# Optimization experiments

Measured on AMD Instinct MI355X. Metric: run time of the kernel, lower is better.

## Reference

```python
import jax, jax.numpy as jnp
import numpy as np

B, S, D, H = 4, 2048, 1024, 16
DK = D // H
THETA = 10000.0


def setup_inputs() -> dict:
    key = jax.random.key(0)
    ks = jax.random.split(key, 5)
    std = (2.0 / (D + D)) ** 0.5  # Linear init std (distribution differs from trunc-normal; math identical)
    x = jax.random.normal(ks[0], (B, S, D), dtype=jnp.float32)
    wq = jax.random.normal(ks[1], (D, D), dtype=jnp.float32) * std
    wk = jax.random.normal(ks[2], (D, D), dtype=jnp.float32) * std
    wv = jax.random.normal(ks[3], (D, D), dtype=jnp.float32) * std
    wo = jax.random.normal(ks[4], (D, D), dtype=jnp.float32) * std
    mask = jnp.tril(jnp.ones((S, S), dtype=bool))  # causal
    return {"x": x, "mask": mask, "wq": wq, "wk": wk, "wv": wv, "wo": wo}


def _rope(t):
    # t: [b, h, s, dk]; interleaved pairs (even, odd)
    s = t.shape[-2]
    inv_freq = THETA ** (-jnp.arange(0, DK, 2, dtype=jnp.float32) / DK)  # [dk/2]
    ang = jnp.arange(s, dtype=jnp.float32)[:, None] * inv_freq[None, :]  # [s, dk/2]
    cos = jnp.cos(ang)[None, None, :, :]
    sin = jnp.sin(ang)[None, None, :, :]
    x1 = t[..., 0::2]
    x2 = t[..., 1::2]
    rot = jnp.stack([x1 * cos - x2 * sin, x1 * sin + x2 * cos], axis=-1)
    return rot.reshape(t.shape)


def reference(x, mask, wq, wk, wv, wo):
    b, s, d = x.shape
    def heads(w):
        return jnp.einsum('bsd,ed->bse', x, w).reshape(b, s, H, DK).transpose(0, 2, 1, 3)
    q = _rope(heads(wq))
    k = _rope(heads(wk))
    v = heads(wv)
    scores = jnp.einsum('bhqd,bhkd->bhqk', q, k) / (DK ** 0.5)
    scores = jnp.where(mask, scores, -jnp.inf)
    attn = jax.nn.softmax(scores, axis=-1)
    out = jnp.einsum('bhqk,bhkd->bhqd', attn, v)
    out = out.transpose(0, 2, 1, 3).reshape(b, s, d)
    return jnp.einsum('bsd,ed->bse', out, wo)
```

## Files before the change

kernel.cpp:

```cpp
#include <hip/hip_runtime.h>

constexpr int Bc = 4, Sc = 2048, Dc = 1024, Hc = 16, DKc = 64;
constexpr int Mc = Bc * Sc;

typedef __bf16 bf16x8 __attribute__((ext_vector_type(8)));
typedef float f32x4 __attribute__((ext_vector_type(4)));
typedef unsigned short ush;

#define DEVI __device__ __forceinline__

DEVI ush bf(float f) { return __builtin_bit_cast(ush, (__bf16)f); }

DEVI void ld_lds16(const void* g, void* l) {
    __builtin_amdgcn_global_load_lds(
        (const __attribute__((address_space(1))) unsigned int*)g,
        (__attribute__((address_space(3))) unsigned int*)l,
        16, 0, 0);
}

constexpr unsigned CVT_BLOCKS = 6144;
constexpr unsigned TAB_BLOCKS = 32;

__global__ __launch_bounds__(256) void cvt_all(
    const float* __restrict__ x,  const float* __restrict__ wq,
    const float* __restrict__ wk, const float* __restrict__ wv,
    const float* __restrict__ wo, ush* __restrict__ dst,
    float2* __restrict__ csn)
{
    if (blockIdx.x >= CVT_BLOCKS) {
        int t = (int)(blockIdx.x - CVT_BLOCKS) * 256 + threadIdx.x;
#pragma unroll
        for (int i = 0; i < 8; i++) {
            int idx = t * 8 + i;
            int s = idx >> 5, p = idx & 31;
            float ang = (float)s * exp2f(-(float)p * 0.4152410118609203f);
            csn[idx] = make_float2(cosf(ang), sinf(ang));
        }
        return;
    }
    size_t t = ((size_t)blockIdx.x * 256 + threadIdx.x) * 8;
    const float* src; size_t loc;
    const size_t NX = (size_t)Mc * Dc;
    if (t < NX) { src = x; loc = t; }
    else {
        size_t u = t - NX;
        int wi = (int)(u >> 20);
        src = (wi == 0) ? wq : ((wi == 1) ? wk : ((wi == 2) ? wv : wo));
        loc = u & 1048575u;
    }
    float4 a = *(const float4*)(src + loc);
    float4 b = *(const float4*)(src + loc + 4);
    union { ush u[8]; float4 v; } o;
    o.u[0] = bf(a.x); o.u[1] = bf(a.y); o.u[2] = bf(a.z); o.u[3] = bf(a.w);
    o.u[4] = bf(b.x); o.u[5] = bf(b.y); o.u[6] = bf(b.z); o.u[7] = bf(b.w);
    *(float4*)(dst + t) = o.v;
}

template<int MODE>
__global__ __launch_bounds__(256) void gemm_bf(
    const ush* __restrict__ A,
    const ush* __restrict__ W0, const ush* __restrict__ W1,
    const ush* __restrict__ W2,
    ush* __restrict__ Oq, ush* __restrict__ Ok, ush* __restrict__ Ovt,
    float* __restrict__ Of, const float2* __restrict__ csn)
{
    __shared__ ush sA[128 * 64];
    __shared__ ush sB[128 * 64];

    const int xcd = (int)blockIdx.x;
    const int u = (int)blockIdx.y + 64 * (int)blockIdx.z;
    const int z = (MODE == 0) ? (u >> 6) : 0;
    const int w = u & 63;
    const int m0 = (xcd * 8 + (w >> 3)) * 128;
    const int n0 = (w & 7) * 128;

    const ush* W = (z == 0) ? W0 : ((z == 1) ? W1 : W2);

    const int tid = threadIdx.x;
    const int wv = tid >> 6;
    const int ln = tid & 63;
    const int lr = ln & 15;
    const int lq = ln >> 4;
    const int wm = (wv & 1) * 64;
    const int wn = (wv >> 1) * 64;
    const int rL = ln >> 3;
    const int cSw = ((ln & 7) ^ rL) * 8;
    const int ca0 = lq ^ (ln & 7);

    f32x4 acc[4][4] = {};
    const bool swp = (MODE == 0) && (z == 2);

    for (int kt = 0; kt < 1024; kt += 64) {
        __syncthreads();
#pragma unroll
        for (int i = 0; i < 4; i++) {
            int chunk = wv * 4 + i;
            int rr = chunk * 8 + rL;
            ld_lds16(&A[(size_t)(m0 + rr) * 1024 + kt + cSw], &sA[chunk * 512]);
            ld_lds16(&W[(size_t)(n0 + rr) * 1024 + kt + cSw], &sB[chunk * 512]);
        }
        __syncthreads();
#pragma unroll
        for (int ks = 0; ks < 2; ks++) {
            const int cf = (ca0 ^ (ks << 2)) << 3;
            bf16x8 af[4], bfr[4];
#pragma unroll
            for (int t = 0; t < 4; t++) {
                af[t]  = *(const bf16x8*)(&sA[(wm + t * 16 + lr) * 64 + cf]);
                bfr[t] = *(const bf16x8*)(&sB[(wn + t * 16 + lr) * 64 + cf]);
            }
            __builtin_amdgcn_s_setprio(1);
            if (!swp) {
#pragma unroll
                for (int mt = 0; mt < 4; mt++)
#pragma unroll
                    for (int nt = 0; nt < 4; nt++)
                        acc[mt][nt] = __builtin_amdgcn_mfma_f32_16x16x32_bf16(
                            af[mt], bfr[nt], acc[mt][nt], 0, 0, 0);
            } else {
#pragma unroll
                for (int mt = 0; mt < 4; mt++)
#pragma unroll
                    for (int nt = 0; nt < 4; nt++)
                        acc[mt][nt] = __builtin_amdgcn_mfma_f32_16x16x32_bf16(
                            bfr[mt], af[nt], acc[mt][nt], 0, 0, 0);
            }
            __builtin_amdgcn_s_setprio(0);
        }
    }

    ush* Oqk = (z == 0) ? Oq : Ok;
#pragma unroll
    for (int mt = 0; mt < 4; mt++) {
#pragma unroll
        for (int nt = 0; nt < 4; nt++) {
#pragma unroll
            for (int r = 0; r < 4; r++) {
                float v = acc[mt][nt][r];
                if (MODE == 1) {
                    int m = m0 + wm + mt * 16 + lq * 4 + r;
                    int n = n0 + wn + nt * 16 + lr;
                    Of[(size_t)m * 1024 + n] = v;
                } else if (swp) {
                    int n = n0 + wn + mt * 16 + lq * 4 + r;
                    int m = m0 + wm + nt * 16 + lr;
                    Ovt[((size_t)((m >> 11) * Hc + (n >> 6)) * DKc + (n & 63)) * Sc
                        + (m & (Sc - 1))] = bf(v);
                } else {
                    int m = m0 + wm + mt * 16 + lq * 4 + r;
                    int n = n0 + wn + nt * 16 + lr;
                    float part = __shfl_xor(v, 1);
                    int dk = n & 63, s = m & (Sc - 1);
                    float2 cs = csn[(s << 5) + (dk >> 1)];
                    float res = (dk & 1) ? (part * cs.y + v * cs.x)
                                         : (v * cs.x - part * cs.y);
                    if (z == 0) res *= 0.18033688011112042f;
                    Oqk[((size_t)((m >> 11) * Hc + (n >> 6)) * Sc + s) * DKc + dk] = bf(res);
                }
            }
        }
    }
}

__global__ __launch_bounds__(256, 2) void attn_k(
    const ush* __restrict__ Q, const ush* __restrict__ Kr,
    const ush* __restrict__ Vt, ush* __restrict__ O)
{
    __shared__ ush kbuf[64 * 72];
    __shared__ ush vbuf[64 * 72];
    __shared__ ush pbuf[4][32 * 76];

    const int head = (int)blockIdx.x * 8 + ((int)blockIdx.y >> 3);
    const int qp   = (int)blockIdx.y & 7;
    const int tid = threadIdx.x;
    const int wv = tid >> 6;
    const int ln = tid & 63;
    const int lr = ln & 15;
    const int lq = ln >> 4;
    const size_t hoff = (size_t)head * Sc * DKc;
    const int rS = tid >> 3;
    const int cS = (tid & 7) * 8;

#define LOADKV(ktv, k0, k1, v0, v1) {                                        \
        int kb_ = (ktv) * 64;                                                \
        k0 = *(const float4*)(&Kr[hoff + (size_t)(kb_ + rS) * DKc + cS]);    \
        k1 = *(const float4*)(&Kr[hoff + (size_t)(kb_ + rS + 32) * DKc + cS]);\
        v0 = *(const float4*)(&Vt[hoff + (size_t)rS * Sc + kb_ + cS]);       \
        v1 = *(const float4*)(&Vt[hoff + (size_t)(rS + 32) * Sc + kb_ + cS]);}

#define WRITEKV(k0, k1, v0, v1) {                                            \
        *(float4*)(&kbuf[rS * 72 + cS]) = k0;                                \
        *(float4*)(&kbuf[(rS + 32) * 72 + cS]) = k1;                         \
        *(float4*)(&vbuf[rS * 72 + cS]) = v0;                                \
        *(float4*)(&vbuf[(rS + 32) * 72 + cS]) = v1; }

#define COMPUTE(ktv) {                                                       \
        const int kb = (ktv) * 64;                                           \
        f32x4 sc[2][4];                                                      \
        __builtin_amdgcn_s_setprio(1);                                       \
        _Pragma("unroll")                                                    \
        for (int nt = 0; nt < 4; nt++) {                                     \
            bf16x8 bk0 = *(const bf16x8*)(&kbuf[(nt * 16 + lr) * 72 + lq * 8]); \
            bf16x8 bk1 = *(const bf16x8*)(&kbuf[(nt * 16 + lr) * 72 + 32 + lq * 8]); \
            _Pragma("unroll")                                                \
            for (int rt = 0; rt < 2; rt++) {                                 \
                f32x4 cc = {};                                               \
                cc = __builtin_amdgcn_mfma_f32_16x16x32_bf16(aq[rt][0], bk0, cc, 0, 0, 0); \
                cc = __builtin_amdgcn_mfma_f32_16x16x32_bf16(aq[rt][1], bk1, cc, 0, 0, 0); \
                sc[rt][nt] = cc;                                             \
            }                                                                \
        }                                                                    \
        __builtin_amdgcn_s_setprio(0);                                       \
        _Pragma("unroll")                                                    \
        for (int rt = 0; rt < 2; rt++) {                                     \
            const int rowmin = qbase + wv * 32 + rt * 16;                    \
            const bool needmask = (kb + 63 > rowmin);                        \
            _Pragma("unroll")                                                \
            for (int nt = 0; nt < 4; nt++) {                                 \
                int col = kb + nt * 16 + lr;                                 \
                _Pragma("unroll")                                            \
                for (int r = 0; r < 4; r++) {                                \
                    float v = sc[rt][nt][r];                                 \
                    if (needmask && col > (rowmin + lq * 4 + r)) v = -1e30f; \
                    float p = exp2f(v);                                      \
                    sc[rt][nt][r] = p;                                       \
                    rs[rt][r] += p;                                          \
                }                                                            \
            }                                                                \
        }                                                                    \
        {                                                                    \
            ush* pb = pbuf[wv];                                              \
            _Pragma("unroll")                                                \
            for (int rt = 0; rt < 2; rt++)                                   \
                _Pragma("unroll")                                            \
                for (int nt = 0; nt < 4; nt++)                               \
                    _Pragma("unroll")                                        \
                    for (int r = 0; r < 4; r++)                              \
                        pb[(rt * 16 + lq * 4 + r) * 76 + nt * 16 + lr] = bf(sc[rt][nt][r]); \
            __builtin_amdgcn_s_setprio(1);                                   \
            _Pragma("unroll")                                                \
            for (int ks = 0; ks < 2; ks++) {                                 \
                bf16x8 ap[2];                                                \
                _Pragma("unroll")                                            \
                for (int rt = 0; rt < 2; rt++)                               \
                    ap[rt] = *(const bf16x8*)(&pb[(rt * 16 + lr) * 76 + ks * 32 + lq * 8]); \
                _Pragma("unroll")                                            \
                for (int nt = 0; nt < 4; nt++) {                             \
                    bf16x8 bv = *(const bf16x8*)(&vbuf[(nt * 16 + lr) * 72 + ks * 32 + lq * 8]); \
                    _Pragma("unroll")                                        \
                    for (int rt = 0; rt < 2; rt++)                           \
                        oacc[rt][nt] = __builtin_amdgcn_mfma_f32_16x16x32_bf16( \
                            ap[rt], bv, oacc[rt][nt], 0, 0, 0);              \
                }                                                            \
            }                                                                \
            __builtin_amdgcn_s_setprio(0);                                   \
        }                                                                    \
    }

    for (int half = 0; half < 2; half++) {
        const int qt = half ? (15 - qp) : qp;
        const int qbase = qt * 128;
        const int kmax = 2 * qt + 2;

        bf16x8 aq[2][2];
#pragma unroll
        for (int rt = 0; rt < 2; rt++) {
            int row = qbase + wv * 32 + rt * 16 + lr;
            const ush* qp_ = &Q[hoff + (size_t)row * DKc + lq * 8];
            aq[rt][0] = *(const bf16x8*)(qp_);
            aq[rt][1] = *(const bf16x8*)(qp_ + 32);
        }

        f32x4 oacc[2][4] = {};
        float rs[2][4] = {};

        float4 ka0, ka1, va0, va1, kb0, kb1, vb0, vb1;

        LOADKV(0, ka0, ka1, va0, va1);
        int kt = 0;
        while (true) {
            __syncthreads();
            WRITEKV(ka0, ka1, va0, va1);
            __syncthreads();
            if (kt + 1 < kmax) LOADKV(kt + 1, kb0, kb1, vb0, vb1);
            COMPUTE(kt);
            kt++;
            if (kt >= kmax) break;
            __syncthreads();
            WRITEKV(kb0, kb1, vb0, vb1);
            __syncthreads();
            if (kt + 1 < kmax) LOADKV(kt + 1, ka0, ka1, va0, va1);
            COMPUTE(kt);
            kt++;
            if (kt >= kmax) break;
        }

        const int b = head >> 4, h = head & 15;
#pragma unroll
        for (int rt = 0; rt < 2; rt++)
#pragma unroll
            for (int r = 0; r < 4; r++) {
                float l = rs[rt][r];
#pragma unroll
                for (int d = 1; d < 16; d <<= 1) l += __shfl_xor(l, d);
                float inv = 1.0f / l;
                int srow = qbase + wv * 32 + rt * 16 + lq * 4 + r;
#pragma unroll
                for (int nt = 0; nt < 4; nt++) {
                    int e = h * 64 + nt * 16 + lr;
                    O[((size_t)(b * Sc + srow)) * Dc + e] = bf(oacc[rt][nt][r] * inv);
                }
            }
    }
#undef LOADKV
#undef WRITEKV
#undef COMPUTE
}

extern "C" void kernel_launch(void* const* d_in, const int* in_sizes, int n_in,
                              void* d_out, int out_size, void* d_ws, size_t ws_size,
                              hipStream_t stream)
{
    (void)in_sizes; (void)n_in; (void)out_size; (void)ws_size;
    const float* x  = (const float*)d_in[0];
    const float* wq = (const float*)d_in[2];
    const float* wk = (const float*)d_in[3];
    const float* wv = (const float*)d_in[4];
    const float* wo = (const float*)d_in[5];

    const size_t N = (size_t)Mc * Dc;
    const size_t NW = (size_t)Dc * Dc;

    ush* xh  = (ush*)d_ws;
    ush* wqh = xh  + N;
    ush* wkh = wqh + NW;
    ush* wvh = wkh + NW;
    ush* woh = wvh + NW;
    ush* vt  = woh + NW;
    ush* ows = vt  + N;
    float2* csn = (float2*)(ows + N);
    ush* qd = (ush*)d_out;
    ush* kd = qd + N;

    cvt_all<<<dim3(CVT_BLOCKS + TAB_BLOCKS), 256, 0, stream>>>(
        x, wq, wk, wv, wo, xh, csn);
    gemm_bf<0><<<dim3(8, 64, 3), 256, 0, stream>>>(
        xh, wqh, wkh, wvh, qd, kd, vt, nullptr, csn);
    attn_k<<<dim3(8, 64), 256, 0, stream>>>(qd, kd, vt, ows);
    gemm_bf<1><<<dim3(8, 64, 1), 256, 0, stream>>>(
        ows, woh, woh, woh, nullptr, nullptr, nullptr, (float*)d_out, csn);
}
```

Baseline: 328.9 us.

## Split attention query tile across 8 waves and XOR-swizzle K/V shared memory

The attention kernel now runs 512 threads per block, and each of 8 waves handles 16 query rows instead of 32, so K/V loads per thread halve and the register footprint shrinks. K and V tiles in LDS drop the padded stride and use an XOR swizzle of 16-byte chunks to avoid bank conflicts. The goal is more waves in flight to hide latency and fewer LDS conflicts. The cost is that each loaded K/V fragment is reused by only one 16-row tile rather than two, which raises LDS read traffic per MFMA.

After: 322.8 us. About the same (-1.9%).

```diff
diff --git a/kernel.cpp b/kernel.cpp
--- a/kernel.cpp
+++ b/kernel.cpp
@@ -162,13 +162,13 @@
     }
 }
 
-__global__ __launch_bounds__(256, 2) void attn_k(
+__global__ __launch_bounds__(512, 4) void attn_k(
     const ush* __restrict__ Q, const ush* __restrict__ Kr,
     const ush* __restrict__ Vt, ush* __restrict__ O)
 {
-    __shared__ ush kbuf[64 * 72];
-    __shared__ ush vbuf[64 * 72];
-    __shared__ ush pbuf[4][32 * 76];
+    __shared__ ush kbuf[64 * 64];
+    __shared__ ush vbuf[64 * 64];
+    __shared__ ush pbuf[8][16 * 76];
 
     const int head = (int)blockIdx.x * 8 + ((int)blockIdx.y >> 3);
     const int qp   = (int)blockIdx.y & 7;
@@ -179,78 +179,66 @@
     const int lq = ln >> 4;
     const size_t hoff = (size_t)head * Sc * DKc;
     const int rS = tid >> 3;
-    const int cS = (tid & 7) * 8;
-
-#define LOADKV(ktv, k0, k1, v0, v1) {                                        \
+    const int c8 = tid & 7;
+    const int cS = c8 * 8;
+    const int cW = ((c8 ^ (rS & 7)) * 8);
+    const int cw0 = ((lq ^ (lr & 7)) * 8);
+
+#define LOADKV(ktv, kk, vv) {                                                \
         int kb_ = (ktv) * 64;                                                \
-        k0 = *(const float4*)(&Kr[hoff + (size_t)(kb_ + rS) * DKc + cS]);    \
-        k1 = *(const float4*)(&Kr[hoff + (size_t)(kb_ + rS + 32) * DKc + cS]);\
-        v0 = *(const float4*)(&Vt[hoff + (size_t)rS * Sc + kb_ + cS]);       \
-        v1 = *(const float4*)(&Vt[hoff + (size_t)(rS + 32) * Sc + kb_ + cS]);}
-
-#define WRITEKV(k0, k1, v0, v1) {                                            \
-        *(float4*)(&kbuf[rS * 72 + cS]) = k0;                                \
-        *(float4*)(&kbuf[(rS + 32) * 72 + cS]) = k1;                         \
-        *(float4*)(&vbuf[rS * 72 + cS]) = v0;                                \
-        *(float4*)(&vbuf[(rS + 32) * 72 + cS]) = v1; }
+        kk = *(const float4*)(&Kr[hoff + (size_t)(kb_ + rS) * DKc + cS]);    \
+        vv = *(const float4*)(&Vt[hoff + (size_t)rS * Sc + kb_ + cS]); }
+
+#define WRITEKV(kk, vv) {                                                    \
+        *(float4*)(&kbuf[rS * 64 + cW]) = kk;                                \
+        *(float4*)(&vbuf[rS * 64 + cW]) = vv; }
 
 #define COMPUTE(ktv) {                                                       \
         const int kb = (ktv) * 64;                                           \
-        f32x4 sc[2][4];                                                      \
+        f32x4 sc[4];                                                         \
         __builtin_amdgcn_s_setprio(1);                                       \
         _Pragma("unroll")                                                    \
         for (int nt = 0; nt < 4; nt++) {                                     \
-            bf16x8 bk0 = *(const bf16x8*)(&kbuf[(nt * 16 + lr) * 72 + lq * 8]); \
-            bf16x8 bk1 = *(const bf16x8*)(&kbuf[(nt * 16 + lr) * 72 + 32 + lq * 8]); \
-            _Pragma("unroll")                                                \
-            for (int rt = 0; rt < 2; rt++) {                                 \
-                f32x4 cc = {};                                               \
-                cc = __builtin_amdgcn_mfma_f32_16x16x32_bf16(aq[rt][0], bk0, cc, 0, 0, 0); \
-                cc = __builtin_amdgcn_mfma_f32_16x16x32_bf16(aq[rt][1], bk1, cc, 0, 0, 0); \
-                sc[rt][nt] = cc;                                             \
-            }                                                                \
+            const ush* kr_ = &kbuf[(nt * 16 + lr) * 64];                     \
+            bf16x8 bk0 = *(const bf16x8*)(kr_ + cw0);                        \
+            bf16x8 bk1 = *(const bf16x8*)(kr_ + (cw0 ^ 32));                 \
+            f32x4 cc = {};                                                   \
+            cc = __builtin_amdgcn_mfma_f32_16x16x32_bf16(aq0, bk0, cc, 0, 0, 0); \
+            cc = __builtin_amdgcn_mfma_f32_16x16x32_bf16(aq1, bk1, cc, 0, 0, 0); \
+            sc[nt] = cc;                                                     \
         }                                                                    \
         __builtin_amdgcn_s_setprio(0);                                       \
+        const int rowq = qbase + wv * 16 + lq * 4;                           \
+        const bool needmask = (kb + 63 > qbase + wv * 16);                   \
         _Pragma("unroll")                                                    \
-        for (int rt = 0; rt < 2; rt++) {                                     \
-            const int rowmin = qbase + wv * 32 + rt * 16;                    \
-            const bool needmask = (kb + 63 > rowmin);                        \
+        for (int nt = 0; nt < 4; nt++) {                                     \
+            int col = kb + nt * 16 + lr;                                     \
             _Pragma("unroll")                                                \
-            for (int nt = 0; nt < 4; nt++) {                                 \
-                int col = kb + nt * 16 + lr;                                 \
-                _Pragma("unroll")                                            \
-                for (int r = 0; r < 4; r++) {                                \
-                    float v = sc[rt][nt][r];                                 \
-                    if (needmask && col > (rowmin + lq * 4 + r)) v = -1e30f; \
-                    float p = exp2f(v);                                      \
-                    sc[rt][nt][r] = p;                                       \
-                    rs[rt][r] += p;                                          \
-                }                                                            \
+            for (int r = 0; r < 4; r++) {                                    \
+                float v = sc[nt][r];                                         \
+                if (needmask && col > rowq + r) v = -1e30f;                  \
+                float p = exp2f(v);                                          \
+                sc[nt][r] = p;                                               \
+                rs[r] += p;                                                  \
             }                                                                \
         }                                                                    \
         {                                                                    \
             ush* pb = pbuf[wv];                                              \
             _Pragma("unroll")                                                \
-            for (int rt = 0; rt < 2; rt++)                                   \
+            for (int nt = 0; nt < 4; nt++)                                   \
                 _Pragma("unroll")                                            \
-                for (int nt = 0; nt < 4; nt++)                               \
-                    _Pragma("unroll")                                        \
-                    for (int r = 0; r < 4; r++)                              \
-                        pb[(rt * 16 + lq * 4 + r) * 76 + nt * 16 + lr] = bf(sc[rt][nt][r]); \
+                for (int r = 0; r < 4; r++)                                  \
+                    pb[(lq * 4 + r) * 76 + nt * 16 + lr] = bf(sc[nt][r]);    \
             __builtin_amdgcn_s_setprio(1);                                   \
             _Pragma("unroll")                                                \
             for (int ks = 0; ks < 2; ks++) {                                 \
-                bf16x8 ap[2];                                                \
-                _Pragma("unroll")                                            \
-                for (int rt = 0; rt < 2; rt++)                               \
-                    ap[rt] = *(const bf16x8*)(&pb[(rt * 16 + lr) * 76 + ks * 32 + lq * 8]); \
+                bf16x8 ap = *(const bf16x8*)(&pb[lr * 76 + ks * 32 + lq * 8]); \
                 _Pragma("unroll")                                            \
                 for (int nt = 0; nt < 4; nt++) {                             \
-                    bf16x8 bv = *(const bf16x8*)(&vbuf[(nt * 16 + lr) * 72 + ks * 32 + lq * 8]); \
-                    _Pragma("unroll")                                        \
-                    for (int rt = 0; rt < 2; rt++)                           \
-                        oacc[rt][nt] = __builtin_amdgcn_mfma_f32_16x16x32_bf16( \
-                            ap[rt], bv, oacc[rt][nt], 0, 0, 0);              \
+                    bf16x8 bv = *(const bf16x8*)(&vbuf[(nt * 16 + lr) * 64   \
+                                                       + (cw0 ^ (ks * 32))]); \
+                    oacc[nt] = __builtin_amdgcn_mfma_f32_16x16x32_bf16(      \
+                        ap, bv, oacc[nt], 0, 0, 0);                          \
                 }                                                            \
             }                                                                \
             __builtin_amdgcn_s_setprio(0);                                   \
@@ -262,34 +250,33 @@
         const int qbase = qt * 128;
         const int kmax = 2 * qt + 2;
 
-        bf16x8 aq[2][2];
-#pragma unroll
-        for (int rt = 0; rt < 2; rt++) {
-            int row = qbase + wv * 32 + rt * 16 + lr;
+        bf16x8 aq0, aq1;
+        {
+            int row = qbase + wv * 16 + lr;
             const ush* qp_ = &Q[hoff + (size_t)row * DKc + lq * 8];
-            aq[rt][0] = *(const bf16x8*)(qp_);
-            aq[rt][1] = *(const bf16x8*)(qp_ + 32);
-        }
-
-        f32x4 oacc[2][4] = {};
-        float rs[2][4] = {};
-
-        float4 ka0, ka1, va0, va1, kb0, kb1, vb0, vb1;
-
-        LOADKV(0, ka0, ka1, va0, va1);
+            aq0 = *(const bf16x8*)(qp_);
+            aq1 = *(const bf16x8*)(qp_ + 32);
+        }
+
+        f32x4 oacc[4] = {};
+        float rs[4] = {};
+
+        float4 ka, va, kb2, vb2;
+
+        LOADKV(0, ka, va);
         int kt = 0;
         while (true) {
             __syncthreads();
-            WRITEKV(ka0, ka1, va0, va1);
+            WRITEKV(ka, va);
             __syncthreads();
-            if (kt + 1 < kmax) LOADKV(kt + 1, kb0, kb1, vb0, vb1);
+            if (kt + 1 < kmax) LOADKV(kt + 1, kb2, vb2);
             COMPUTE(kt);
             kt++;
             if (kt >= kmax) break;
             __syncthreads();
-            WRITEKV(kb0, kb1, vb0, vb1);
+            WRITEKV(kb2, vb2);
             __syncthreads();
-            if (kt + 1 < kmax) LOADKV(kt + 1, ka0, ka1, va0, va1);
+            if (kt + 1 < kmax) LOADKV(kt + 1, ka, va);
             COMPUTE(kt);
             kt++;
             if (kt >= kmax) break;
@@ -297,20 +284,18 @@
 
         const int b = head >> 4, h = head & 15;
 #pragma unroll
-        for (int rt = 0; rt < 2; rt++)
-#pragma unroll
-            for (int r = 0; r < 4; r++) {
-                float l = rs[rt][r];
-#pragma unroll
-                for (int d = 1; d < 16; d <<= 1) l += __shfl_xor(l, d);
-                float inv = 1.0f / l;
-                int srow = qbase + wv * 32 + rt * 16 + lq * 4 + r;
-#pragma unroll
-                for (int nt = 0; nt < 4; nt++) {
-                    int e = h * 64 + nt * 16 + lr;
-                    O[((size_t)(b * Sc + srow)) * Dc + e] = bf(oacc[rt][nt][r] * inv);
-                }
+        for (int r = 0; r < 4; r++) {
+            float l = rs[r];
+#pragma unroll
+            for (int d = 1; d < 16; d <<= 1) l += __shfl_xor(l, d);
+            float inv = 1.0f / l;
+            int srow = qbase + wv * 16 + lq * 4 + r;
+#pragma unroll
+            for (int nt = 0; nt < 4; nt++) {
+                int e = h * 64 + nt * 16 + lr;
+                O[((size_t)(b * Sc + srow)) * Dc + e] = bf(oacc[nt][r] * inv);
             }
+        }
     }
 #undef LOADKV
 #undef WRITEKV
@@ -346,7 +331,7 @@
         x, wq, wk, wv, wo, xh, csn);
     gemm_bf<0><<<dim3(8, 64, 3), 256, 0, stream>>>(
         xh, wqh, wkh, wvh, qd, kd, vt, nullptr, csn);
-    attn_k<<<dim3(8, 64), 256, 0, stream>>>(qd, kd, vt, ows);
+    attn_k<<<dim3(8, 64), 512, 0, stream>>>(qd, kd, vt, ows);
     gemm_bf<1><<<dim3(8, 64, 1), 256, 0, stream>>>(
         ows, woh, woh, woh, nullptr, nullptr, nullptr, (float*)d_out, csn);
 }
```
